# Performance work log

Hardware: AMD Instinct MI355X
Metric: run time of the kernel (lower is better)

The kernel has to match this reference:

```python
import jax, jax.numpy as jnp
import numpy as np

N_NODES = 100000
N_EDGES = 1600000
D_FEAT = 128
HIDDEN = 256
N_CLASSES = 40


def setup_inputs() -> dict:
    key = jax.random.key(0)
    ks = jax.random.split(key, 6)
    x = jax.random.normal(ks[0], (N_NODES, D_FEAT), dtype=jnp.float32)
    edge_index = jax.random.randint(ks[1], (2, N_EDGES), 0, N_NODES, dtype=jnp.int32)
    # Glorot-ish scaled weights
    w1_l = jax.random.normal(ks[2], (HIDDEN, D_FEAT), dtype=jnp.float32) / np.sqrt(D_FEAT)
    w1_r = jax.random.normal(ks[3], (HIDDEN, D_FEAT), dtype=jnp.float32) / np.sqrt(D_FEAT)
    w2_l = jax.random.normal(ks[4], (N_CLASSES, HIDDEN), dtype=jnp.float32) / np.sqrt(HIDDEN)
    w2_r = jax.random.normal(ks[5], (N_CLASSES, HIDDEN), dtype=jnp.float32) / np.sqrt(HIDDEN)
    b1_l = jnp.zeros((HIDDEN,), jnp.float32)
    b2_l = jnp.zeros((N_CLASSES,), jnp.float32)
    return {"x": x, "edge_index": edge_index, "w1_l": w1_l, "b1_l": b1_l,
            "w1_r": w1_r, "w2_l": w2_l, "b2_l": b2_l, "w2_r": w2_r}


def _sage_conv(x, src, dst, n_nodes, w_l, b_l, w_r):
    # mean aggregation of source-node features onto target nodes
    msg = x[src]                                                  # [E, d]
    agg = jax.ops.segment_sum(msg, dst, num_segments=n_nodes)     # [N, d]
    cnt = jax.ops.segment_sum(jnp.ones((dst.shape[0], 1), x.dtype), dst,
                              num_segments=n_nodes)               # [N, 1]
    agg = agg / jnp.maximum(cnt, 1.0)
    # out = lin_l(agg) + lin_r(x); lin_l has bias, lin_r does not (PyG default)
    return agg @ w_l.T + b_l + x @ w_r.T


def reference(x, edge_index, w1_l, b1_l, w1_r, w2_l, b2_l, w2_r):
    n_nodes = x.shape[0]
    src, dst = edge_index[0], edge_index[1]
    h = jax.nn.relu(_sage_conv(x, src, dst, n_nodes, w1_l, b1_l, w1_r))
    # dropout is identity in eval mode
    out = _sage_conv(h, src, dst, n_nodes, w2_l, b2_l, w2_r)
    return jax.nn.log_softmax(out, axis=1)
```

## Files before the change

kernel.cpp:

```cpp
#include <hip/hip_runtime.h>
#include <hip/hip_bf16.h>
#include <stdint.h>

#define NN 100000
#define NE 1600000
#define DF 128
#define DH 256
#define NC 40
#define BSHIFT 8
#define NBKT 391
#define EPB 8192
#define NBIN_BLOCKS ((NE + EPB - 1) / EPB)

typedef __attribute__((ext_vector_type(8))) short short8;
typedef __attribute__((ext_vector_type(4))) float f32x4;

typedef const __attribute__((address_space(1))) unsigned int* gas1;
typedef __attribute__((address_space(3))) unsigned int* las3;

__device__ __forceinline__ void gload16(const void* g, void* l) {
  __builtin_amdgcn_global_load_lds((gas1)g, (las3)l, 16, 0, 0);
}

__device__ __forceinline__ unsigned short f2bf(float f) {
  union { float f; unsigned u; } v; v.f = f;
  unsigned r = v.u + 0x7FFFu + ((v.u >> 16) & 1u);
  return (unsigned short)(r >> 16);
}
__device__ __forceinline__ float bflo(unsigned u) {
  union { unsigned u; float f; } v; v.u = u << 16; return v.f;
}
__device__ __forceinline__ float bfhi(unsigned u) {
  union { unsigned u; float f; } v; v.u = u & 0xFFFF0000u; return v.f;
}

__global__ void k_xbf16(const float* __restrict__ x, unsigned* __restrict__ xb) {
  int i = blockIdx.x * blockDim.x + threadIdx.x;
  if (i < NN * 64) {
    float2 v = ((const float2*)x)[i];
    xb[i] = ((unsigned)f2bf(v.y) << 16) | f2bf(v.x);
  }
}

__global__ __launch_bounds__(256) void k_bhist(const int* __restrict__ dst, int* __restrict__ bcnt) {
  __shared__ int h[NBKT];
  int tid = threadIdx.x;
  for (int b = tid; b < NBKT; b += 256) h[b] = 0;
  __syncthreads();
  int base = blockIdx.x * EPB;
  int n = NE - base; if (n > EPB) n = EPB;
  for (int i = tid; i < n; i += 256) atomicAdd(&h[dst[base + i] >> BSHIFT], 1);
  __syncthreads();
  for (int b = tid; b < NBKT; b += 256) if (h[b]) atomicAdd(&bcnt[b], h[b]);
}

__global__ __launch_bounds__(512) void k_bscan(const int* __restrict__ bcnt,
                                               int* __restrict__ boff, int* __restrict__ bcur) {
  __shared__ int s[512];
  int tid = threadIdx.x;
  int v = (tid < NBKT) ? bcnt[tid] : 0;
  s[tid] = v;
  __syncthreads();
  for (int off = 1; off < 512; off <<= 1) {
    int a = (tid >= off) ? s[tid - off] : 0;
    __syncthreads();
    s[tid] += a;
    __syncthreads();
  }
  int excl = s[tid] - v;
  if (tid < NBKT) { boff[tid] = excl; bcur[tid] = excl; }
  if (tid == 0) boff[NBKT] = s[511];
}

__global__ __launch_bounds__(256) void k_bin(const int* __restrict__ src, const int* __restrict__ dst,
                                             int* __restrict__ bcur, unsigned* __restrict__ pairs) {
  __shared__ int hcnt[NBKT];
  __shared__ int hbase[NBKT];
  int tid = threadIdx.x;
  for (int b = tid; b < NBKT; b += 256) hcnt[b] = 0;
  __syncthreads();
  int base = blockIdx.x * EPB;
  int n = NE - base; if (n > EPB) n = EPB;
  for (int i = tid; i < n; i += 256) atomicAdd(&hcnt[dst[base + i] >> BSHIFT], 1);
  __syncthreads();
  for (int b = tid; b < NBKT; b += 256) hbase[b] = hcnt[b] ? atomicAdd(&bcur[b], hcnt[b]) : 0;
  __syncthreads();
  for (int b = tid; b < NBKT; b += 256) hcnt[b] = 0;
  __syncthreads();
  for (int i = tid; i < n; i += 256) {
    int s = src[base + i], d = dst[base + i];
    int b = d >> BSHIFT;
    int slot = atomicAdd(&hcnt[b], 1);
    pairs[hbase[b] + slot] = (unsigned)s | ((unsigned)(d & 255) << 17);
  }
}

__global__ __launch_bounds__(256) void k_csr(const unsigned* __restrict__ pairs,
                                             const int* __restrict__ boff,
                                             int* __restrict__ row_ptr, int* __restrict__ csr) {
  __shared__ int ncnt[256];
  __shared__ int noff[256];
  int tid = threadIdx.x;
  int b = blockIdx.x;
  int base = boff[b], end = boff[b + 1];
  ncnt[tid] = 0;
  __syncthreads();
  for (int e = base + tid; e < end; e += 256) atomicAdd(&ncnt[pairs[e] >> 17], 1);
  __syncthreads();
  int v = ncnt[tid];
  noff[tid] = v;
  __syncthreads();
  for (int off = 1; off < 256; off <<= 1) {
    int a = (tid >= off) ? noff[tid - off] : 0;
    __syncthreads();
    noff[tid] += a;
    __syncthreads();
  }
  int excl = noff[tid] - v;
  __syncthreads();
  noff[tid] = excl;
  ncnt[tid] = 0;
  __syncthreads();
  int gnode = (b << BSHIFT) + tid;
  if (gnode < NN) row_ptr[gnode] = base + excl;
  if (b == NBKT - 1 && tid == 0) row_ptr[NN] = NE;
  for (int e = base + tid; e < end; e += 256) {
    unsigned p = pairs[e];
    int ld = p >> 17;
    int slot = atomicAdd(&ncnt[ld], 1);
    csr[base + noff[ld] + slot] = (int)(p & 0x1FFFFu);
  }
}

__global__ void k_packw(const float* __restrict__ w1l, const float* __restrict__ w1r,
                        const float* __restrict__ w2l, const float* __restrict__ w2r,
                        unsigned short* __restrict__ Wc, unsigned short* __restrict__ W2c) {
  int i = blockIdx.x * blockDim.x + threadIdx.x;
  if (i < 256 * 256) {
    int o = i >> 8, k = i & 255;
    float v = (k < 128) ? w1l[o * 128 + k] : w1r[o * 128 + (k - 128)];
    Wc[i] = f2bf(v);
  }
  int j = i - 256 * 256;
  if (j >= 0 && j < 80 * 256) {
    int o = j >> 8, k = j & 255;
    float v = (o < 40) ? w2l[o * 256 + k] : w2r[(o - 40) * 256 + k];
    W2c[j] = f2bf(v);
  }
}

__global__ void k_agg1(const unsigned* __restrict__ xb, const int* __restrict__ row_ptr,
                       const int* __restrict__ csr_src, unsigned* __restrict__ A1) {
  int w = threadIdx.x >> 6, lane = threadIdx.x & 63;
  int node = blockIdx.x * 4 + w;
  if (node >= NN) return;
  int rs = row_ptr[node], re = row_ptr[node + 1];
  float a0 = 0.f, a1 = 0.f;
  for (int e = rs; e < re; e += 8) {
    unsigned v[8];
#pragma unroll
    for (int j = 0; j < 8; ++j) {
      int ej = e + j;
      int idx = csr_src[ej < re ? ej : re - 1];
      unsigned t = xb[(size_t)idx * 64 + lane];
      v[j] = (ej < re) ? t : 0u;
    }
#pragma unroll
    for (int j = 0; j < 8; ++j) { a0 += bflo(v[j]); a1 += bfhi(v[j]); }
  }
  int deg = re - rs;
  float inv = 1.f / (float)(deg > 0 ? deg : 1);
  unsigned pack = ((unsigned)f2bf(a1 * inv) << 16) | f2bf(a0 * inv);
  A1[(size_t)node * 64 + lane] = pack;
}

__global__ __launch_bounds__(512) void k_gemm1(const unsigned short* __restrict__ A1,
                                               const unsigned short* __restrict__ XB,
                                               const unsigned short* __restrict__ Wc,
                                               const float* __restrict__ b1,
                                               unsigned short* __restrict__ H) {
  __shared__ __align__(16) unsigned short sA[128 * 64];
  __shared__ __align__(16) unsigned short sB[256 * 64];
  int tid = threadIdx.x;
  int w = tid >> 6, lane = tid & 63;
  int brow = blockIdx.x * 128;
  int wr = (w >> 1) * 32, wc = (w & 1) * 128;
  f32x4 acc[2][8] = {};

  for (int kt = 0; kt < 4; ++kt) {
    const unsigned short* srcA = (kt < 2) ? A1 : XB;
    int kcol = (kt & 1) * 64;
#pragma unroll
    for (int t = 0; t < 2; ++t) {
      int c = t * 512 + tid;
      int r = c >> 3, cc = c & 7;
      int scc = cc ^ (r & 7);
      int gr = brow + r; if (gr > NN - 1) gr = NN - 1;
      gload16(srcA + (size_t)gr * 128 + kcol + scc * 8, sA + c * 8);
    }
#pragma unroll
    for (int t = 0; t < 4; ++t) {
      int c = t * 512 + tid;
      int r = c >> 3, cc = c & 7;
      int scc = cc ^ (r & 7);
      gload16(Wc + (size_t)r * 256 + kt * 64 + scc * 8, sB + c * 8);
    }
    __syncthreads();
#pragma unroll
    for (int kg = 0; kg < 2; ++kg) {
      short8 af[2], bfr[8];
#pragma unroll
      for (int m = 0; m < 2; ++m) {
        int row = wr + m * 16 + (lane & 15);
        int cch = (kg * 4 + (lane >> 4)) ^ (row & 7);
        af[m] = *(const short8*)(sA + row * 64 + cch * 8);
      }
#pragma unroll
      for (int n = 0; n < 8; ++n) {
        int row = wc + n * 16 + (lane & 15);
        int cch = (kg * 4 + (lane >> 4)) ^ (row & 7);
        bfr[n] = *(const short8*)(sB + row * 64 + cch * 8);
      }
#pragma unroll
      for (int m = 0; m < 2; ++m)
#pragma unroll
        for (int n = 0; n < 8; ++n)
          acc[m][n] = __builtin_amdgcn_mfma_f32_16x16x32_bf16(af[m], bfr[n], acc[m][n], 0, 0, 0);
    }
    __syncthreads();
  }

  int colbase = wc + (lane & 15);
  int rowbase = brow + wr + (lane >> 4) * 4;
#pragma unroll
  for (int n = 0; n < 8; ++n) {
    int col = colbase + n * 16;
    float bias = b1[col];
#pragma unroll
    for (int m = 0; m < 2; ++m) {
      int row0 = rowbase + m * 16;
#pragma unroll
      for (int q = 0; q < 4; ++q) {
        int row = row0 + q;
        if (row < NN) {
          float v = acc[m][n][q] + bias;
          v = v > 0.f ? v : 0.f;
          H[(size_t)row * 256 + col] = f2bf(v);
        }
      }
    }
  }
}

__global__ __launch_bounds__(256) void k_gemm2(const unsigned short* __restrict__ H,
                                               const unsigned short* __restrict__ W2c,
                                               unsigned short* __restrict__ Pb,
                                               float* __restrict__ R) {
  __shared__ __align__(16) unsigned short sA[128 * 64];
  __shared__ __align__(16) unsigned short sB[80 * 64];
  int tid = threadIdx.x;
  int w = tid >> 6, lane = tid & 63;
  int brow = blockIdx.x * 128;
  f32x4 acc[2][5] = {};

  for (int kt = 0; kt < 4; ++kt) {
#pragma unroll
    for (int t = 0; t < 4; ++t) {
      int c = (t * 4 + w) * 64 + lane;
      int r = c >> 3, cc = c & 7;
      int scc = cc ^ (r & 7);
      int gr = brow + r; if (gr > NN - 1) gr = NN - 1;
      gload16(H + (size_t)gr * 256 + kt * 64 + scc * 8, sA + c * 8);
    }
    for (int g = w; g < 10; g += 4) {
      int c = g * 64 + lane;
      int r = c >> 3, cc = c & 7;
      int scc = cc ^ (r & 7);
      gload16(W2c + (size_t)r * 256 + kt * 64 + scc * 8, sB + c * 8);
    }
    __syncthreads();
#pragma unroll
    for (int kg = 0; kg < 2; ++kg) {
      short8 af[2], bfr[5];
#pragma unroll
      for (int m = 0; m < 2; ++m) {
        int row = w * 32 + m * 16 + (lane & 15);
        int cch = (kg * 4 + (lane >> 4)) ^ (row & 7);
        af[m] = *(const short8*)(sA + row * 64 + cch * 8);
      }
#pragma unroll
      for (int n = 0; n < 5; ++n) {
        int row = n * 16 + (lane & 15);
        int cch = (kg * 4 + (lane >> 4)) ^ (row & 7);
        bfr[n] = *(const short8*)(sB + row * 64 + cch * 8);
      }
#pragma unroll
      for (int m = 0; m < 2; ++m)
#pragma unroll
        for (int n = 0; n < 5; ++n)
          acc[m][n] = __builtin_amdgcn_mfma_f32_16x16x32_bf16(af[m], bfr[n], acc[m][n], 0, 0, 0);
    }
    __syncthreads();
  }

  int colbase = lane & 15;
  int rowbase = brow + w * 32 + (lane >> 4) * 4;
#pragma unroll
  for (int m = 0; m < 2; ++m) {
#pragma unroll
    for (int n = 0; n < 5; ++n) {
      int col = colbase + n * 16;
#pragma unroll
      for (int q = 0; q < 4; ++q) {
        int row = rowbase + m * 16 + q;
        if (row < NN) {
          float v = acc[m][n][q];
          if (col < NC) Pb[(size_t)row * 64 + col] = f2bf(v);
          else {
            R[(size_t)row * NC + (col - NC)] = v;
            if (col < 64) Pb[(size_t)row * 64 + col] = 0;
          }
        }
      }
    }
  }
}

__global__ __launch_bounds__(256) void k_final(const unsigned short* __restrict__ Pb,
                                               const float* __restrict__ R,
                                               const int* __restrict__ row_ptr,
                                               const int* __restrict__ csr_src,
                                               const float* __restrict__ b2,
                                               float* __restrict__ out) {
  int w = threadIdx.x >> 6, lane = threadIdx.x & 63;
  int g = lane >> 4, r = lane & 15;
  int node = blockIdx.x * 4 + w;
  if (node >= NN) return;
  int rs = row_ptr[node], re = row_ptr[node + 1];
  float s0 = 0.f, s1 = 0.f, s2 = 0.f, s3 = 0.f;
  int nfull = (re - rs) >> 3;
  int e = rs + g;
  for (int it = 0; it < nfull; ++it, e += 8) {
    int sa = csr_src[e];
    int sb = csr_src[e + 4];
    uint2 va = *(const uint2*)(Pb + (size_t)sa * 64 + r * 4);
    uint2 vb = *(const uint2*)(Pb + (size_t)sb * 64 + r * 4);
    s0 += bflo(va.x) + bflo(vb.x);
    s1 += bfhi(va.x) + bfhi(vb.x);
    s2 += bflo(va.y) + bflo(vb.y);
    s3 += bfhi(va.y) + bfhi(vb.y);
  }
  if (e < re) {
    int sa = csr_src[e];
    uint2 va = *(const uint2*)(Pb + (size_t)sa * 64 + r * 4);
    s0 += bflo(va.x); s1 += bfhi(va.x); s2 += bflo(va.y); s3 += bfhi(va.y);
  }
  e += 4;
  if (e < re) {
    int sa = csr_src[e];
    uint2 va = *(const uint2*)(Pb + (size_t)sa * 64 + r * 4);
    s0 += bflo(va.x); s1 += bfhi(va.x); s2 += bflo(va.y); s3 += bfhi(va.y);
  }
  s0 += __shfl_xor(s0, 16); s0 += __shfl_xor(s0, 32);
  s1 += __shfl_xor(s1, 16); s1 += __shfl_xor(s1, 32);
  s2 += __shfl_xor(s2, 16); s2 += __shfl_xor(s2, 32);
  s3 += __shfl_xor(s3, 16); s3 += __shfl_xor(s3, 32);

  int deg = re - rs;
  float inv = 1.f / (float)(deg > 0 ? deg : 1);
  bool act = r < 10;
  float4 rr = act ? *(const float4*)(R + (size_t)node * NC + r * 4) : make_float4(0, 0, 0, 0);
  float4 bb = act ? *(const float4*)(b2 + r * 4) : make_float4(0, 0, 0, 0);
  float v0 = s0 * inv + rr.x + bb.x;
  float v1 = s1 * inv + rr.y + bb.y;
  float v2 = s2 * inv + rr.z + bb.z;
  float v3 = s3 * inv + rr.w + bb.w;
  float mx = act ? fmaxf(fmaxf(v0, v1), fmaxf(v2, v3)) : -1e30f;
#pragma unroll
  for (int o = 1; o < 16; o <<= 1) mx = fmaxf(mx, __shfl_xor(mx, o));
  float ex = act ? (__expf(v0 - mx) + __expf(v1 - mx) + __expf(v2 - mx) + __expf(v3 - mx)) : 0.f;
#pragma unroll
  for (int o = 1; o < 16; o <<= 1) ex += __shfl_xor(ex, o);
  float ls = mx + __logf(ex);
  if (g == 0 && act) {
    float4 o4 = make_float4(v0 - ls, v1 - ls, v2 - ls, v3 - ls);
    *(float4*)(out + (size_t)node * NC + r * 4) = o4;
  }
}

extern "C" void kernel_launch(void* const* d_in, const int* in_sizes, int n_in,
                              void* d_out, int out_size, void* d_ws, size_t ws_size,
                              hipStream_t stream) {
  const float* x   = (const float*)d_in[0];
  const int*   ei  = (const int*)d_in[1];
  const float* w1l = (const float*)d_in[2];
  const float* b1  = (const float*)d_in[3];
  const float* w1r = (const float*)d_in[4];
  const float* w2l = (const float*)d_in[5];
  const float* b2  = (const float*)d_in[6];
  const float* w2r = (const float*)d_in[7];
  float* out = (float*)d_out;
  const int* src = ei;
  const int* dst = ei + NE;

  char* ws = (char*)d_ws;
  size_t off = 0;
  auto alloc = [&](size_t bytes) -> char* {
    char* p = ws + off;
    off = (off + bytes + 255) & ~(size_t)255;
    return p;
  };
  int* bcnt     = (int*)alloc((size_t)(NBKT + 1) * 4);
  int* boff     = (int*)alloc((size_t)(NBKT + 1) * 4);
  int* bcur     = (int*)alloc((size_t)NBKT * 4);
  int* row_ptr  = (int*)alloc((size_t)(NN + 1) * 4);
  unsigned* pairs = (unsigned*)alloc((size_t)NE * 4);
  int* csr      = (int*)alloc((size_t)NE * 4);
  unsigned short* Wc  = (unsigned short*)alloc(256 * 256 * 2);
  unsigned short* W2c = (unsigned short*)alloc(80 * 256 * 2);
  unsigned*       xb  = (unsigned*)alloc((size_t)NN * 64 * 4);
  unsigned*       A1  = (unsigned*)alloc((size_t)NN * 64 * 4);
  unsigned short* H   = (unsigned short*)alloc((size_t)NN * 256 * 2);
  unsigned short* Pb  = (unsigned short*)alloc((size_t)NN * 64 * 2);
  float*          R   = (float*)alloc((size_t)NN * NC * 4);

  hipMemsetAsync(bcnt, 0, (size_t)(NBKT + 1) * 4, stream);
  k_bhist<<<NBIN_BLOCKS, 256, 0, stream>>>(dst, bcnt);
  k_xbf16<<<(NN * 64 + 255) / 256, 256, 0, stream>>>(x, xb);
  k_bscan<<<1, 512, 0, stream>>>(bcnt, boff, bcur);
  k_bin<<<NBIN_BLOCKS, 256, 0, stream>>>(src, dst, bcur, pairs);
  k_csr<<<NBKT, 256, 0, stream>>>(pairs, boff, row_ptr, csr);
  k_packw<<<336, 256, 0, stream>>>(w1l, w1r, w2l, w2r, Wc, W2c);
  k_agg1<<<(NN + 3) / 4, 256, 0, stream>>>(xb, row_ptr, csr, A1);
  k_gemm1<<<(NN + 127) / 128, 512, 0, stream>>>((const unsigned short*)A1,
                                                (const unsigned short*)xb, Wc, b1, H);
  k_gemm2<<<(NN + 127) / 128, 256, 0, stream>>>(H, W2c, Pb, R);
  k_final<<<(NN + 3) / 4, 256, 0, stream>>>(Pb, R, row_ptr, csr, b2, out);
}
```

Before: 362.3 us.

## Fuse layer-1 and layer-2 GEMMs, keeping hidden activations in shared memory

Merges the first GEMM (with bias and ReLU) and the second projection GEMM into one kernel. Each block of 64 rows writes its bf16 hidden tile to swizzled LDS and then multiplies it by the packed layer-2 weights, using the hidden tile as the B operand. This removes the global write and re-read of the 100000x256 hidden matrix. In exchange the block uses about 72KB of LDS with smaller row tiles, which may lower occupancy and reuse of the layer-1 weights, and the output stores are vectorized.

```diff
diff --git a/kernel.cpp b/kernel.cpp
--- a/kernel.cpp
+++ b/kernel.cpp
@@ -174,16 +174,19 @@
   A1[(size_t)node * 64 + lane] = pack;
 }
 
-__global__ __launch_bounds__(512) void k_gemm1(const unsigned short* __restrict__ A1,
+__global__ __launch_bounds__(256) void k_fused(const unsigned short* __restrict__ A1,
                                                const unsigned short* __restrict__ XB,
                                                const unsigned short* __restrict__ Wc,
                                                const float* __restrict__ b1,
-                                               unsigned short* __restrict__ H) {
-  __shared__ __align__(16) unsigned short sA[128 * 64];
+                                               const unsigned short* __restrict__ W2c,
+                                               unsigned short* __restrict__ Pb,
+                                               float* __restrict__ R) {
+  __shared__ __align__(16) unsigned short sA[64 * 64];
   __shared__ __align__(16) unsigned short sB[256 * 64];
+  __shared__ __align__(16) unsigned short sH[64 * 256];
   int tid = threadIdx.x;
   int w = tid >> 6, lane = tid & 63;
-  int brow = blockIdx.x * 128;
+  int brow = blockIdx.x * 64;
   int wr = (w >> 1) * 32, wc = (w & 1) * 128;
   f32x4 acc[2][8] = {};
 
@@ -192,15 +195,15 @@
     int kcol = (kt & 1) * 64;
 #pragma unroll
     for (int t = 0; t < 2; ++t) {
-      int c = t * 512 + tid;
+      int c = t * 256 + tid;
       int r = c >> 3, cc = c & 7;
       int scc = cc ^ (r & 7);
       int gr = brow + r; if (gr > NN - 1) gr = NN - 1;
       gload16(srcA + (size_t)gr * 128 + kcol + scc * 8, sA + c * 8);
     }
 #pragma unroll
-    for (int t = 0; t < 4; ++t) {
-      int c = t * 512 + tid;
+    for (int t = 0; t < 8; ++t) {
+      int c = t * 256 + tid;
       int r = c >> 3, cc = c & 7;
       int scc = cc ^ (r & 7);
       gload16(Wc + (size_t)r * 256 + kt * 64 + scc * 8, sB + c * 8);
@@ -230,97 +233,74 @@
     __syncthreads();
   }
 
-  int colbase = wc + (lane & 15);
-  int rowbase = brow + wr + (lane >> 4) * 4;
-#pragma unroll
-  for (int n = 0; n < 8; ++n) {
-    int col = colbase + n * 16;
-    float bias = b1[col];
-#pragma unroll
-    for (int m = 0; m < 2; ++m) {
-      int row0 = rowbase + m * 16;
-#pragma unroll
-      for (int q = 0; q < 4; ++q) {
-        int row = row0 + q;
-        if (row < NN) {
+  {
+    int colbase = wc + (lane & 15);
+    int rowb = wr + (lane >> 4) * 4;
+#pragma unroll
+    for (int n = 0; n < 8; ++n) {
+      int col = colbase + n * 16;
+      float bias = b1[col];
+      int g = col >> 3, off = col & 7;
+#pragma unroll
+      for (int m = 0; m < 2; ++m) {
+        int row0 = rowb + m * 16;
+#pragma unroll
+        for (int q = 0; q < 4; ++q) {
+          int row = row0 + q;
           float v = acc[m][n][q] + bias;
           v = v > 0.f ? v : 0.f;
-          H[(size_t)row * 256 + col] = f2bf(v);
+          sH[row * 256 + ((g ^ (row & 7)) << 3) + off] = f2bf(v);
         }
       }
     }
   }
-}
-
-__global__ __launch_bounds__(256) void k_gemm2(const unsigned short* __restrict__ H,
-                                               const unsigned short* __restrict__ W2c,
-                                               unsigned short* __restrict__ Pb,
-                                               float* __restrict__ R) {
-  __shared__ __align__(16) unsigned short sA[128 * 64];
-  __shared__ __align__(16) unsigned short sB[80 * 64];
-  int tid = threadIdx.x;
-  int w = tid >> 6, lane = tid & 63;
-  int brow = blockIdx.x * 128;
-  f32x4 acc[2][5] = {};
-
+  __syncthreads();
+
+  f32x4 a2[5] = {};
+  int nrow = w * 16 + (lane & 15);
   for (int kt = 0; kt < 4; ++kt) {
 #pragma unroll
-    for (int t = 0; t < 4; ++t) {
-      int c = (t * 4 + w) * 64 + lane;
-      int r = c >> 3, cc = c & 7;
-      int scc = cc ^ (r & 7);
-      int gr = brow + r; if (gr > NN - 1) gr = NN - 1;
-      gload16(H + (size_t)gr * 256 + kt * 64 + scc * 8, sA + c * 8);
-    }
-    for (int g = w; g < 10; g += 4) {
-      int c = g * 64 + lane;
-      int r = c >> 3, cc = c & 7;
-      int scc = cc ^ (r & 7);
-      gload16(W2c + (size_t)r * 256 + kt * 64 + scc * 8, sB + c * 8);
+    for (int t = 0; t < 3; ++t) {
+      int c = t * 256 + tid;
+      if (c < 640) {
+        int r = c >> 3, cc = c & 7;
+        int scc = cc ^ (r & 7);
+        gload16(W2c + (size_t)r * 256 + kt * 64 + scc * 8, sB + c * 8);
+      }
     }
     __syncthreads();
 #pragma unroll
     for (int kg = 0; kg < 2; ++kg) {
-      short8 af[2], bfr[5];
-#pragma unroll
-      for (int m = 0; m < 2; ++m) {
-        int row = w * 32 + m * 16 + (lane & 15);
-        int cch = (kg * 4 + (lane >> 4)) ^ (row & 7);
-        af[m] = *(const short8*)(sA + row * 64 + cch * 8);
-      }
-#pragma unroll
-      for (int n = 0; n < 5; ++n) {
-        int row = n * 16 + (lane & 15);
-        int cch = (kg * 4 + (lane >> 4)) ^ (row & 7);
-        bfr[n] = *(const short8*)(sB + row * 64 + cch * 8);
-      }
-#pragma unroll
-      for (int m = 0; m < 2; ++m)
-#pragma unroll
-        for (int n = 0; n < 5; ++n)
-          acc[m][n] = __builtin_amdgcn_mfma_f32_16x16x32_bf16(af[m], bfr[n], acc[m][n], 0, 0, 0);
-    }
-    __syncthreads();
-  }
-
-  int colbase = lane & 15;
-  int rowbase = brow + w * 32 + (lane >> 4) * 4;
-#pragma unroll
-  for (int m = 0; m < 2; ++m) {
-#pragma unroll
-    for (int n = 0; n < 5; ++n) {
-      int col = colbase + n * 16;
-#pragma unroll
-      for (int q = 0; q < 4; ++q) {
-        int row = rowbase + m * 16 + q;
-        if (row < NN) {
-          float v = acc[m][n][q];
-          if (col < NC) Pb[(size_t)row * 64 + col] = f2bf(v);
-          else {
-            R[(size_t)row * NC + (col - NC)] = v;
-            if (col < 64) Pb[(size_t)row * 64 + col] = 0;
-          }
-        }
+      int gH = kt * 8 + kg * 4 + (lane >> 4);
+      short8 bf1 = *(const short8*)(sH + nrow * 256 + ((gH ^ (nrow & 7)) << 3));
+      short8 af[5];
+#pragma unroll
+      for (int m = 0; m < 5; ++m) {
+        int arow = m * 16 + (lane & 15);
+        int cch = (kg * 4 + (lane >> 4)) ^ (arow & 7);
+        af[m] = *(const short8*)(sB + arow * 64 + cch * 8);
+      }
+#pragma unroll
+      for (int m = 0; m < 5; ++m)
+        a2[m] = __builtin_amdgcn_mfma_f32_16x16x32_bf16(af[m], bf1, a2[m], 0, 0, 0);
+    }
+    __syncthreads();
+  }
+
+  int node = brow + nrow;
+  if (node < NN) {
+#pragma unroll
+    for (int m = 0; m < 5; ++m) {
+      int c0 = m * 16 + (lane >> 4) * 4;
+      f32x4 v = a2[m];
+      if (c0 < NC) {
+        uint2 pk;
+        pk.x = ((unsigned)f2bf(v[1]) << 16) | f2bf(v[0]);
+        pk.y = ((unsigned)f2bf(v[3]) << 16) | f2bf(v[2]);
+        *(uint2*)(Pb + (size_t)node * 64 + c0) = pk;
+      } else {
+        if (c0 < 64) *(uint2*)(Pb + (size_t)node * 64 + c0) = make_uint2(0u, 0u);
+        *(float4*)(R + (size_t)node * NC + (c0 - NC)) = make_float4(v[0], v[1], v[2], v[3]);
       }
     }
   }
@@ -420,7 +400,6 @@
   unsigned short* W2c = (unsigned short*)alloc(80 * 256 * 2);
   unsigned*       xb  = (unsigned*)alloc((size_t)NN * 64 * 4);
   unsigned*       A1  = (unsigned*)alloc((size_t)NN * 64 * 4);
-  unsigned short* H   = (unsigned short*)alloc((size_t)NN * 256 * 2);
   unsigned short* Pb  = (unsigned short*)alloc((size_t)NN * 64 * 2);
   float*          R   = (float*)alloc((size_t)NN * NC * 4);
 
@@ -432,8 +411,7 @@
   k_csr<<<NBKT, 256, 0, stream>>>(pairs, boff, row_ptr, csr);
   k_packw<<<336, 256, 0, stream>>>(w1l, w1r, w2l, w2r, Wc, W2c);
   k_agg1<<<(NN + 3) / 4, 256, 0, stream>>>(xb, row_ptr, csr, A1);
-  k_gemm1<<<(NN + 127) / 128, 512, 0, stream>>>((const unsigned short*)A1,
-                                                (const unsigned short*)xb, Wc, b1, H);
-  k_gemm2<<<(NN + 127) / 128, 256, 0, stream>>>(H, W2c, Pb, R);
+  k_fused<<<(NN + 63) / 64, 256, 0, stream>>>((const unsigned short*)A1,
+                                              (const unsigned short*)xb, Wc, b1, W2c, Pb, R);
   k_final<<<(NN + 3) / 4, 256, 0, stream>>>(Pb, R, row_ptr, csr, b2, out);
 }
```

Measured after the change: 323.4 us. 10.8% less time.
